# Performance work log

Measured on AMD Instinct MI355X. Metric: run time of the kernel, lower is better.

Reference implementation:

```python
import jax, jax.numpy as jnp
import numpy as np

B, S, D, H = 4, 2048, 768, 12
DK = D // H


def setup_inputs() -> dict:
    key = jax.random.key(0)
    ks = jax.random.split(key, 12)
    scale = 1.0 / np.sqrt(D)
    inp = {
        "q": jax.random.normal(ks[0], (B, S, D), jnp.float32),
        "k": jax.random.normal(ks[1], (B, S, D), jnp.float32),
        "v": jax.random.normal(ks[2], (B, S, D), jnp.float32),
        # True = masked position (broadcast over heads and query positions)
        "mask": jax.random.randint(ks[3], (B, 1, 1, S), 0, 2).astype(bool),
        "Wq": jax.random.normal(ks[4], (D, D), jnp.float32) * scale,
        "bq": jnp.zeros((D,), jnp.float32),
        "Wk": jax.random.normal(ks[5], (D, D), jnp.float32) * scale,
        "bk": jnp.zeros((D,), jnp.float32),
        "Wv": jax.random.normal(ks[6], (D, D), jnp.float32) * scale,
        "bv": jnp.zeros((D,), jnp.float32),
        "Wo": jax.random.normal(ks[7], (D, D), jnp.float32) * scale,
        "bo": jnp.zeros((D,), jnp.float32),
    }
    return inp


def _split_heads(x):
    # [B, S, D] -> [B, H, S, DK]
    b, s, _ = x.shape
    return x.reshape(b, s, H, DK).transpose(0, 2, 1, 3)


def reference(q, k, v, mask, Wq, bq, Wk, bk, Wv, bv, Wo, bo):
    qh = _split_heads(q @ Wq + bq)
    kh = _split_heads(k @ Wk + bk)
    vh = _split_heads(v @ Wv + bv)
    # unfused scaled-dot-product attention: full [B,H,S,S] scores
    score = jnp.einsum("bhqd,bhkd->bhqk", qh, kh) / jnp.sqrt(jnp.float32(DK))
    neg = jnp.finfo(score.dtype).min
    score = jnp.where(mask, neg, score)
    attn = jax.nn.softmax(score, axis=-1)  # dropout p=0 (eval) -> identity
    ctx = jnp.einsum("bhqk,bhkd->bhqd", attn, vh)
    ctx = ctx.transpose(0, 2, 1, 3).reshape(q.shape[0], -1, D)
    return ctx @ Wo + bo
```

## Files before the change

### kernel.cpp

```cpp
#include <hip/hip_runtime.h>

#define Bn 4
#define Sn 2048
#define Dn 768
#define Hn 12
#define DKn 64
#define Mn (Bn * Sn)

typedef __bf16 bf16x8 __attribute__((ext_vector_type(8)));
typedef float f32x4 __attribute__((ext_vector_type(4)));

static __device__ __forceinline__ float4 ld4(const float* p) { return *(const float4*)p; }

static __device__ __forceinline__ f32x4 mfma16(bf16x8 a, bf16x8 b, f32x4 c) {
  return __builtin_amdgcn_mfma_f32_16x16x32_bf16(a, b, c, 0, 0, 0);
}

static __device__ __forceinline__ void glds16(const void* g, void* l) {
  __builtin_amdgcn_global_load_lds(
      (const __attribute__((address_space(1))) unsigned int*)(uintptr_t)g,
      (__attribute__((address_space(3))) unsigned int*)(unsigned int)(uintptr_t)l, 16, 0, 0);
}

static __device__ __forceinline__ bf16x8 ldsfrag(const __bf16* base, int row, int kbyte) {
  const char* p = (const char*)base + row * 128 + (kbyte ^ ((row & 7) << 4));
  return *(const bf16x8*)p;
}

static __device__ __forceinline__ void lds_w16(__bf16* base, int row, int col, __bf16 v) {
  char* p = (char*)base + row * 128 + ((col * 2) ^ ((row & 7) << 4));
  *(__bf16*)p = v;
}

static __device__ __forceinline__ bf16x8 cvt8(float4 a, float4 b) {
  bf16x8 o;
  o[0] = (__bf16)a.x; o[1] = (__bf16)a.y; o[2] = (__bf16)a.z; o[3] = (__bf16)a.w;
  o[4] = (__bf16)b.x; o[5] = (__bf16)b.y; o[6] = (__bf16)b.z; o[7] = (__bf16)b.w;
  return o;
}

__global__ __launch_bounds__(256) void prep_kernel(
    const unsigned char* __restrict__ mask,
    const float* __restrict__ Wq, const float* __restrict__ Wk,
    const float* __restrict__ Wv, const float* __restrict__ Wo,
    __bf16* __restrict__ Wt, int* __restrict__ cidx, int* __restrict__ nbp) {
  const int t = threadIdx.x;
  const int bid = blockIdx.x;

  if (bid < 144) {
    __shared__ __bf16 T[64][72];
    const int zi = bid / 36;
    const int rem = bid % 36;
    const int bx = rem % 6, by = rem / 6;
    const float* W = zi == 0 ? Wq : zi == 1 ? Wk : zi == 2 ? Wv : Wo;
    __bf16* out = Wt + (size_t)zi * Dn * Dn;
    const int k0 = bx * 128, n0 = by * 128;
#pragma unroll
    for (int sk = 0; sk < 2; ++sk)
#pragma unroll
      for (int sn = 0; sn < 2; ++sn) {
        const int kk0 = k0 + sk * 64, nn0 = n0 + sn * 64;
        __syncthreads();
#pragma unroll
        for (int i = 0; i < 4; ++i) {
          int flat = t + i * 256;
          int row = flat >> 4;
          int c4 = (flat & 15) * 4;
          float4 vv = ld4(&W[(size_t)(kk0 + row) * Dn + nn0 + c4]);
          T[c4 + 0][row] = (__bf16)vv.x;
          T[c4 + 1][row] = (__bf16)vv.y;
          T[c4 + 2][row] = (__bf16)vv.z;
          T[c4 + 3][row] = (__bf16)vv.w;
        }
        __syncthreads();
#pragma unroll
        for (int i = 0; i < 2; ++i) {
          int flat = t + i * 256;
          int row = flat >> 3;
          int c8 = (flat & 7) * 8;
          *(bf16x8*)&out[(size_t)(nn0 + row) * Dn + kk0 + c8] = *(bf16x8*)&T[row][c8];
        }
      }
    return;
  }

  __shared__ int dcnt;
  __shared__ int cnts[256];
  __shared__ int offs[256];
  const int b = bid - 144;
  if (t == 0) dcnt = 0;
  __syncthreads();
  int c = 0;
#pragma unroll
  for (int i = 0; i < 32; ++i) c += (mask[t * 32 + i] != 0) ? 1 : 0;
  atomicAdd(&dcnt, c);
  __syncthreads();
  const int mflag = dcnt > 2457;
  const unsigned char* m8 = mask + (size_t)b * Sn;
  const int* m32 = (const int*)mask + (size_t)b * Sn;
  bool um[8];
  int lc = 0;
#pragma unroll
  for (int i = 0; i < 8; ++i) {
    const int s = t * 8 + i;
    const bool masked = mflag ? (m8[s] != 0) : (m32[s] != 0);
    um[i] = !masked;
    lc += um[i] ? 1 : 0;
  }
  cnts[t] = lc;
  __syncthreads();
  if (t == 0) {
    int acc = 0;
    for (int i = 0; i < 256; ++i) {
      offs[i] = acc;
      acc += cnts[i];
    }
    nbp[b] = acc;
  }
  __syncthreads();
  int o = offs[t];
  int* out = cidx + (size_t)b * Sn;
#pragma unroll
  for (int i = 0; i < 8; ++i)
    if (um[i]) out[o++] = t * 8 + i;
}

__global__ __launch_bounds__(256) void convert_kernel(
    const float* __restrict__ q, const float* __restrict__ k, const float* __restrict__ v,
    const int* __restrict__ cidx, const int* __restrict__ nbp,
    __bf16* __restrict__ qb, __bf16* __restrict__ kb, __bf16* __restrict__ vb) {
  const int t = threadIdx.x;
  const int z = blockIdx.z;
  const int bid = blockIdx.x;

  if (z == 0) {
    if (bid >= 3072) return;
    size_t i = ((size_t)bid * 256 + t) * 8;
    *(bf16x8*)(qb + i) = cvt8(ld4(q + i), ld4(q + i + 4));
    return;
  }
  if (t >= 192) return;
  const float* src = z == 1 ? k : v;
  __bf16* dst = z == 1 ? kb : vb;
  const int b = bid >> 10;
  const int i = ((bid & 1023) << 1) + (t / 96);
  const int c8 = (t % 96) * 8;
  const int nb = nbp[b];
  __bf16* orow = dst + ((size_t)b * Sn + i) * Dn + c8;
  if (i < nb) {
    const int s = cidx[b * Sn + i];
    const float* irow = src + ((size_t)b * Sn + s) * Dn + c8;
    *(bf16x8*)orow = cvt8(ld4(irow), ld4(irow + 4));
  } else {
    bf16x8 zz = {};
    *(bf16x8*)orow = zz;
  }
}

template <int MODE>
static __device__ __forceinline__ void gemm_mfma_core(__bf16* __restrict__ As,
                                                      __bf16* __restrict__ Bs,
                                                      const __bf16* __restrict__ X,
                                                      const __bf16* __restrict__ Bt,
                                                      const float* __restrict__ bias,
                                                      void* __restrict__ Y) {
  const int tid = threadIdx.x;
  const int lane = tid & 63;
  const int wave = __builtin_amdgcn_readfirstlane(tid >> 6);
  const int l15 = lane & 15, lq = lane >> 4;
  const int m0 = blockIdx.x * 128, n0 = blockIdx.y * 128;
  const int wr = wave >> 1, wc = wave & 1;

  f32x4 acc[4][4];
#pragma unroll
  for (int i = 0; i < 4; ++i)
#pragma unroll
    for (int j = 0; j < 4; ++j) acc[i][j] = (f32x4){0.f, 0.f, 0.f, 0.f};

  for (int kt = 0; kt < Dn / 64; ++kt) {
    __syncthreads();
#pragma unroll
    for (int i = 0; i < 4; ++i) {
      int r0 = (i * 4 + wave) * 8;
      int row = r0 + (lane >> 3);
      int chunk = (lane & 7) ^ (row & 7);
      glds16(X + (size_t)(m0 + row) * Dn + kt * 64 + chunk * 8, As + r0 * 64);
      glds16(Bt + (size_t)(n0 + row) * Dn + kt * 64 + chunk * 8, Bs + r0 * 64);
    }
    __syncthreads();
#pragma unroll
    for (int kk = 0; kk < 2; ++kk) {
      bf16x8 a[4], b[4];
#pragma unroll
      for (int i = 0; i < 4; ++i) a[i] = ldsfrag(As, wr * 64 + i * 16 + l15, kk * 64 + lq * 16);
#pragma unroll
      for (int j = 0; j < 4; ++j) b[j] = ldsfrag(Bs, wc * 64 + j * 16 + l15, kk * 64 + lq * 16);
#pragma unroll
      for (int i = 0; i < 4; ++i)
#pragma unroll
        for (int j = 0; j < 4; ++j) acc[i][j] = mfma16(a[i], b[j], acc[i][j]);
    }
  }

#pragma unroll
  for (int i = 0; i < 4; ++i)
#pragma unroll
    for (int j = 0; j < 4; ++j) {
      const int gcol = n0 + wc * 64 + j * 16 + l15;
      const float bv = bias[gcol];
#pragma unroll
      for (int r = 0; r < 4; ++r) {
        const int grow = m0 + wr * 64 + i * 16 + lq * 4 + r;
        const float val = acc[i][j][r] + bv;
        if (MODE == 0) {
          const int b = grow >> 11, s = grow & (Sn - 1);
          const int h = gcol >> 6, dk = gcol & 63;
          ((__bf16*)Y)[(((size_t)b * Hn + h) * Sn + s) * DKn + dk] = (__bf16)val;
        } else if (MODE == 2) {
          const int b = grow >> 11, s = grow & (Sn - 1);
          const int h = gcol >> 6, dk = gcol & 63;
          ((__bf16*)Y)[(((size_t)b * Hn + h) * DKn + dk) * Sn + s] = (__bf16)val;
        } else {
          ((float*)Y)[(size_t)grow * Dn + gcol] = val;
        }
      }
    }
}

__global__ __launch_bounds__(256, 4) void qkv_gemm_mfma_kernel(
    const __bf16* __restrict__ qb, const __bf16* __restrict__ kb, const __bf16* __restrict__ vb,
    const __bf16* __restrict__ Wt, const int* __restrict__ nbp,
    const float* __restrict__ bq, const float* __restrict__ bk, const float* __restrict__ bv,
    __bf16* __restrict__ qh, __bf16* __restrict__ kh, __bf16* __restrict__ vht) {
  __shared__ __bf16 As[128 * 64];
  __shared__ __bf16 Bs[128 * 64];
  const int z = blockIdx.z;
  if (z != 0) {
    const int m0 = blockIdx.x * 128;
    const int b = m0 >> 11, ml = m0 & (Sn - 1);
    const int lim = (nbp[b] + 127) & ~127;
    if (ml >= lim) return;
  }
  if (z == 0) {
    gemm_mfma_core<0>(As, Bs, qb, Wt, bq, qh);
  } else if (z == 1) {
    gemm_mfma_core<0>(As, Bs, kb, Wt + (size_t)Dn * Dn, bk, kh);
  } else {
    gemm_mfma_core<2>(As, Bs, vb, Wt + 2 * (size_t)Dn * Dn, bv, vht);
  }
}

__global__ __launch_bounds__(256, 4) void out_gemm_mfma_kernel(const __bf16* __restrict__ ctxb,
                                                               const __bf16* __restrict__ Wot,
                                                               const float* __restrict__ bo,
                                                               float* __restrict__ out) {
  __shared__ __bf16 As[128 * 64];
  __shared__ __bf16 Bs[128 * 64];
  gemm_mfma_core<1>(As, Bs, ctxb, Wot, bo, out);
}

__global__ __launch_bounds__(256, 3) void attn_mfma_kernel(
    const __bf16* __restrict__ qh, const __bf16* __restrict__ kh, const __bf16* __restrict__ vht,
    const int* __restrict__ nbp, __bf16* __restrict__ ctxb) {
  __shared__ __bf16 QPs[128 * 64];
  __shared__ __bf16 KVs[4][64 * 64];
  const int tid = threadIdx.x;
  const int lane = tid & 63;
  const int wave = __builtin_amdgcn_readfirstlane(tid >> 6);
  const int l15 = lane & 15, lq = lane >> 4;
  const int q0 = blockIdx.x * 128;
  const int bh = blockIdx.y;
  const int b = bh / Hn, h = bh % Hn;
  const int nb = nbp[b];
  const int NT = (nb + 63) >> 6;
  const __bf16* Qg = qh + (size_t)bh * Sn * DKn;
  const __bf16* Kg = kh + (size_t)bh * Sn * DKn;
  const __bf16* Vg = vht + (size_t)bh * DKn * Sn;
  const float C1 = 0.18033688011112042f;
  const float C2 = -23.083120654223414f;

  auto stageKV = [&](int t, int buf) {
#pragma unroll
    for (int i = 0; i < 2; ++i) {
      int r0 = wave * 16 + i * 8;
      int row = r0 + (lane >> 3);
      int chunk = (lane & 7) ^ (row & 7);
      glds16(Kg + (size_t)(t * 64 + row) * DKn + chunk * 8, (__bf16*)KVs[buf] + r0 * 64);
      glds16(Vg + (size_t)row * Sn + t * 64 + chunk * 8, (__bf16*)KVs[2 + buf] + r0 * 64);
    }
  };

#pragma unroll
  for (int i = 0; i < 4; ++i) {
    int r0 = wave * 32 + i * 8;
    int row = r0 + (lane >> 3);
    int chunk = (lane & 7) ^ (row & 7);
    glds16(Qg + (size_t)(q0 + row) * DKn + chunk * 8, (__bf16*)QPs + r0 * 64);
  }
  stageKV(0, 0);
  __syncthreads();

  bf16x8 aq[2][2];
#pragma unroll
  for (int qb = 0; qb < 2; ++qb)
#pragma unroll
    for (int kk = 0; kk < 2; ++kk)
      aq[qb][kk] = ldsfrag(QPs, wave * 32 + qb * 16 + l15, kk * 64 + lq * 16);

  f32x4 ctx[2][4];
  float lsum[2][4];
#pragma unroll
  for (int qb = 0; qb < 2; ++qb)
#pragma unroll
    for (int j = 0; j < 4; ++j) {
      ctx[qb][j] = (f32x4){0.f, 0.f, 0.f, 0.f};
      lsum[qb][j] = 0.f;
    }

  int cur = 0;
  for (int t = 0; t < NT; ++t) {
    if (t + 1 < NT) stageKV(t + 1, cur ^ 1);

    f32x4 sc[2][4];
#pragma unroll
    for (int qb = 0; qb < 2; ++qb)
#pragma unroll
      for (int j = 0; j < 4; ++j) sc[qb][j] = (f32x4){0.f, 0.f, 0.f, 0.f};
#pragma unroll
    for (int kk = 0; kk < 2; ++kk)
#pragma unroll
      for (int j = 0; j < 4; ++j) {
        bf16x8 bk = ldsfrag(KVs[cur], j * 16 + l15, kk * 64 + lq * 16);
        sc[0][j] = mfma16(aq[0][kk], bk, sc[0][j]);
        sc[1][j] = mfma16(aq[1][kk], bk, sc[1][j]);
      }

    if (t != NT - 1) {
#pragma unroll
      for (int qb = 0; qb < 2; ++qb)
#pragma unroll
        for (int j = 0; j < 4; ++j)
#pragma unroll
          for (int r = 0; r < 4; ++r) {
            const float p = __builtin_amdgcn_exp2f(fmaf(sc[qb][j][r], C1, C2));
            lsum[qb][r] += p;
            lds_w16(QPs, wave * 32 + qb * 16 + lq * 4 + r, j * 16 + l15, (__bf16)p);
          }
    } else {
      const int limit = nb - t * 64;
      bool live[4];
#pragma unroll
      for (int j = 0; j < 4; ++j) live[j] = (j * 16 + l15) < limit;
#pragma unroll
      for (int qb = 0; qb < 2; ++qb)
#pragma unroll
        for (int j = 0; j < 4; ++j)
#pragma unroll
          for (int r = 0; r < 4; ++r) {
            float p = __builtin_amdgcn_exp2f(fmaf(sc[qb][j][r], C1, C2));
            p = live[j] ? p : 0.f;
            lsum[qb][r] += p;
            lds_w16(QPs, wave * 32 + qb * 16 + lq * 4 + r, j * 16 + l15, (__bf16)p);
          }
    }

    bf16x8 pa[2][2];
#pragma unroll
    for (int qb = 0; qb < 2; ++qb)
#pragma unroll
      for (int kk = 0; kk < 2; ++kk)
        pa[qb][kk] = ldsfrag(QPs, wave * 32 + qb * 16 + l15, kk * 64 + lq * 16);
#pragma unroll
    for (int kk = 0; kk < 2; ++kk)
#pragma unroll
      for (int j = 0; j < 4; ++j) {
        bf16x8 bv = ldsfrag(KVs[2 + cur], j * 16 + l15, kk * 64 + lq * 16);
        ctx[0][j] = mfma16(pa[0][kk], bv, ctx[0][j]);
        ctx[1][j] = mfma16(pa[1][kk], bv, ctx[1][j]);
      }

    __syncthreads();
    cur ^= 1;
  }

#pragma unroll
  for (int sh = 1; sh <= 8; sh <<= 1)
#pragma unroll
    for (int qb = 0; qb < 2; ++qb)
#pragma unroll
      for (int r = 0; r < 4; ++r) lsum[qb][r] += __shfl_xor(lsum[qb][r], sh, 64);

#pragma unroll
  for (int qb = 0; qb < 2; ++qb)
#pragma unroll
    for (int r = 0; r < 4; ++r) {
      const float inv = 1.0f / lsum[qb][r];
      const int s = q0 + wave * 32 + qb * 16 + lq * 4 + r;
#pragma unroll
      for (int j = 0; j < 4; ++j) {
        const int col = h * DKn + j * 16 + l15;
        ctxb[((size_t)b * Sn + s) * Dn + col] = (__bf16)(ctx[qb][j][r] * inv);
      }
    }
}

extern "C" void kernel_launch(void* const* d_in, const int* in_sizes, int n_in,
                              void* d_out, int out_size, void* d_ws, size_t ws_size,
                              hipStream_t stream) {
  const float* q = (const float*)d_in[0];
  const float* k = (const float*)d_in[1];
  const float* v = (const float*)d_in[2];
  const unsigned char* mask = (const unsigned char*)d_in[3];
  const float* Wq = (const float*)d_in[4];
  const float* bq = (const float*)d_in[5];
  const float* Wk = (const float*)d_in[6];
  const float* bk = (const float*)d_in[7];
  const float* Wv = (const float*)d_in[8];
  const float* bv = (const float*)d_in[9];
  const float* Wo = (const float*)d_in[10];
  const float* bo = (const float*)d_in[11];
  float* out = (float*)d_out;

  char* base = (char*)d_ws;
  const size_t XB = (size_t)Mn * Dn * 2;
  const size_t WT = (size_t)Dn * Dn * 2;
  __bf16* qb = (__bf16*)(base);
  __bf16* kb = (__bf16*)(base + XB);
  __bf16* vb = (__bf16*)(base + 2 * XB);
  __bf16* Wt = (__bf16*)(base + 3 * XB);
  __bf16* qh = (__bf16*)(base + 3 * XB + 4 * WT);
  __bf16* kh = (__bf16*)(base + 4 * XB + 4 * WT);
  __bf16* vht = (__bf16*)(base + 5 * XB + 4 * WT);
  int* cidx = (int*)(base + 6 * XB + 4 * WT);
  int* nbp = cidx + Bn * Sn;
  __bf16* ctxb = kb;

  prep_kernel<<<148, 256, 0, stream>>>(mask, Wq, Wk, Wv, Wo, Wt, cidx, nbp);
  convert_kernel<<<dim3(4096, 1, 3), 256, 0, stream>>>(q, k, v, cidx, nbp, qb, kb, vb);
  qkv_gemm_mfma_kernel<<<dim3(Mn / 128, Dn / 128, 3), 256, 0, stream>>>(
      qb, kb, vb, Wt, nbp, bq, bk, bv, qh, kh, vht);
  attn_mfma_kernel<<<dim3(Sn / 128, Bn * Hn), 256, 0, stream>>>(qh, kh, vht, nbp, ctxb);
  out_gemm_mfma_kernel<<<dim3(Mn / 128, Dn / 128), 256, 0, stream>>>(ctxb, Wt + 3 * (size_t)Dn * Dn,
                                                                     bo, out);
}
```

Before: 119.2 us.

## Pack softmax probabilities into 8-byte LDS stores with permuted V key order

The softmax P tile is now written to LDS as packed bf16 pairs (v_cvt_pk_bf16_f32), one 8-byte store per row per lane instead of 16 scalar 2-byte stores. The key dimension of P is permuted so that each lane's four columns sit next to each other. To match, the transposed V output of the QKV GEMM stores its sequence index with the same permutation within each 64-key block, keeping the P·V contraction consistent. The masked and unmasked paths are also merged into one loop with a live predicate, which adds per-element selects on every tile.

```diff
diff --git a/kernel.cpp b/kernel.cpp
--- a/kernel.cpp
+++ b/kernel.cpp
@@ -16,6 +16,12 @@
   return __builtin_amdgcn_mfma_f32_16x16x32_bf16(a, b, c, 0, 0, 0);
 }
 
+static __device__ __forceinline__ unsigned int cvtpk(float lo, float hi) {
+  unsigned int r;
+  asm("v_cvt_pk_bf16_f32 %0, %1, %2" : "=v"(r) : "v"(lo), "v"(hi));
+  return r;
+}
+
 static __device__ __forceinline__ void glds16(const void* g, void* l) {
   __builtin_amdgcn_global_load_lds(
       (const __attribute__((address_space(1))) unsigned int*)(uintptr_t)g,
@@ -25,11 +31,6 @@
 static __device__ __forceinline__ bf16x8 ldsfrag(const __bf16* base, int row, int kbyte) {
   const char* p = (const char*)base + row * 128 + (kbyte ^ ((row & 7) << 4));
   return *(const bf16x8*)p;
-}
-
-static __device__ __forceinline__ void lds_w16(__bf16* base, int row, int col, __bf16 v) {
-  char* p = (char*)base + row * 128 + ((col * 2) ^ ((row & 7) << 4));
-  *(__bf16*)p = v;
 }
 
 static __device__ __forceinline__ bf16x8 cvt8(float4 a, float4 b) {
@@ -219,7 +220,8 @@
         } else if (MODE == 2) {
           const int b = grow >> 11, s = grow & (Sn - 1);
           const int h = gcol >> 6, dk = gcol & 63;
-          ((__bf16*)Y)[(((size_t)b * Hn + h) * DKn + dk) * Sn + s] = (__bf16)val;
+          const int sp = (s & ~63) | ((s & 15) << 2) | ((s >> 4) & 3);
+          ((__bf16*)Y)[(((size_t)b * Hn + h) * DKn + dk) * Sn + sp] = (__bf16)val;
         } else {
           ((float*)Y)[(size_t)grow * Dn + gcol] = val;
         }
@@ -335,34 +337,29 @@
         sc[1][j] = mfma16(aq[1][kk], bk, sc[1][j]);
       }
 
-    if (t != NT - 1) {
-#pragma unroll
-      for (int qb = 0; qb < 2; ++qb)
-#pragma unroll
-        for (int j = 0; j < 4; ++j)
-#pragma unroll
-          for (int r = 0; r < 4; ++r) {
-            const float p = __builtin_amdgcn_exp2f(fmaf(sc[qb][j][r], C1, C2));
-            lsum[qb][r] += p;
-            lds_w16(QPs, wave * 32 + qb * 16 + lq * 4 + r, j * 16 + l15, (__bf16)p);
-          }
-    } else {
-      const int limit = nb - t * 64;
-      bool live[4];
-#pragma unroll
-      for (int j = 0; j < 4; ++j) live[j] = (j * 16 + l15) < limit;
-#pragma unroll
-      for (int qb = 0; qb < 2; ++qb)
-#pragma unroll
-        for (int j = 0; j < 4; ++j)
-#pragma unroll
-          for (int r = 0; r < 4; ++r) {
-            float p = __builtin_amdgcn_exp2f(fmaf(sc[qb][j][r], C1, C2));
-            p = live[j] ? p : 0.f;
-            lsum[qb][r] += p;
-            lds_w16(QPs, wave * 32 + qb * 16 + lq * 4 + r, j * 16 + l15, (__bf16)p);
-          }
-    }
+    const bool lastt = (t == NT - 1);
+    const int limit = nb - t * 64;
+    bool live[4];
+#pragma unroll
+    for (int j = 0; j < 4; ++j) live[j] = !lastt || ((j * 16 + l15) < limit);
+#pragma unroll
+    for (int qb = 0; qb < 2; ++qb)
+#pragma unroll
+      for (int r = 0; r < 4; ++r) {
+        float p[4];
+#pragma unroll
+        for (int j = 0; j < 4; ++j) {
+          float pv = __builtin_amdgcn_exp2f(fmaf(sc[qb][j][r], C1, C2));
+          p[j] = live[j] ? pv : 0.f;
+          lsum[qb][r] += p[j];
+        }
+        uint2 w;
+        w.x = cvtpk(p[0], p[1]);
+        w.y = cvtpk(p[2], p[3]);
+        const int row = wave * 32 + qb * 16 + lq * 4 + r;
+        char* dst = (char*)QPs + row * 128 + ((l15 * 8) ^ ((row & 7) << 4));
+        *(uint2*)dst = w;
+      }
 
     bf16x8 pa[2][2];
 #pragma unroll
```

Result: faster. 113.7 us, median of 2 (-4.6%).
